# Optimization experiments

Hardware: AMD Instinct MI355X
Metric: run time of the kernel (lower is better)

The kernel has to match this reference:

```python
import jax, jax.numpy as jnp
import numpy as np
from jax import lax

SEQ, BS, D_IN, D_H, D_OUT, N_LAYERS = 784, 256, 1, 512, 1, 3

def _glorot(key, shape):
    fan_in, fan_out = shape[0], shape[1]
    std = jnp.sqrt(2.0 / (fan_in + fan_out))
    return (jax.random.normal(key, shape) * std).astype(jnp.float32)

def setup_inputs() -> dict:
    key = jax.random.key(0)
    ks = jax.random.split(key, 3 + 3 * N_LAYERS + 2)
    x = jax.random.normal(ks[0], (SEQ, BS, D_IN), dtype=jnp.float32)
    W0 = _glorot(ks[1], (D_IN, D_H))
    b0 = jnp.zeros((D_H,), jnp.float32)
    # per-layer recurrence params, stacked: a (L,D_H), B (L,D_H,D_H), C (L,D_H,D_H)
    a = jnp.stack([jax.random.uniform(ks[2 + i], (D_H,), minval=0.999, maxval=1.001) for i in range(N_LAYERS)]).astype(jnp.float32)
    B = jnp.stack([_glorot(ks[2 + N_LAYERS + i], (D_H, D_H)) for i in range(N_LAYERS)])
    C = jnp.stack([_glorot(ks[2 + 2 * N_LAYERS + i], (D_H, D_H)) for i in range(N_LAYERS)])
    Wf = _glorot(ks[2 + 3 * N_LAYERS], (D_H, D_OUT))
    bf = jnp.zeros((D_OUT,), jnp.float32)
    return {"x": x, "W0": W0, "b0": b0, "a": a, "B": B, "C": C, "Wf": Wf, "bf": bf}

def _rnn_layer(x, a_l, B_l, C_l):
    # x: (seq, bs, d_h); diagonal linear recurrence h_t = h_{t-1} * a + x_t @ B
    xb = jnp.einsum('sbi,ih->sbh', x, B_l)  # precompute input projection
    def step(h, xt):
        h = h * a_l + xt
        return h, h
    _, hs = lax.scan(step, jnp.zeros((x.shape[1], a_l.shape[0]), x.dtype), xb)
    return jnp.einsum('sbh,ho->sbo', hs, C_l)

def reference(x, W0, b0, a, B, C, Wf, bf):
    identity = x  # use_downsampling=False, use_residual=True
    h = jax.nn.relu(x @ W0 + b0)
    for l in range(N_LAYERS):
        h = jax.nn.relu(_rnn_layer(h, a[l], B[l], C[l]))
    out = h @ Wf + bf
    return out + identity
```

## Files before the change

kernel.cpp:

```cpp
#include <hip/hip_runtime.h>
#include <hip/hip_bf16.h>

#define SEQ 784
#define BS  256
#define DH  512
#define MT  (SEQ * BS)
#define NL  3
#define NC  14
#define CL  56
#define COLS (BS * DH)

typedef unsigned short u16;
typedef __bf16  bf16x8  __attribute__((ext_vector_type(8)));
typedef float   f32x4   __attribute__((ext_vector_type(4)));
typedef unsigned short u16x8 __attribute__((ext_vector_type(8)));
typedef unsigned short u16x4 __attribute__((ext_vector_type(4)));

__device__ __forceinline__ u16 f2b(float f) {
    unsigned int x = __float_as_uint(f);
    unsigned int r = (x + 0x7FFFu + ((x >> 16) & 1u)) >> 16;
    return (u16)r;
}
__device__ __forceinline__ float b2f(u16 u) {
    return __uint_as_float(((unsigned int)u) << 16);
}

__global__ __launch_bounds__(256) void prep_k(const float* __restrict__ B,
                                              const float* __restrict__ C,
                                              u16* __restrict__ Bp,
                                              u16* __restrict__ Cp)
{
    const long t = (long)blockIdx.x * 256 + threadIdx.x;
    const int  e  = (int)(t & 7);
    const int  l  = (int)((t >> 3) & 63);
    const int  ni = (int)((t >> 9) & 3);
    const int  wd = (int)((t >> 11) & 7);
    const int  g  = (int)((t >> 14) & 15);
    const long lay = t >> 18;
    const int  n = wd * 64 + ni * 16 + (l & 15);
    const int  k = g * 32 + (l >> 4) * 8 + e;
    const long src = (lay << 18) + (long)k * DH + n;
    Bp[t] = f2b(B[src]);
    Cp[t] = f2b(C[src]);
}


#define GEMM_STEP_KK(ATILE, tt)                                                  \
    _Pragma("unroll")                                                            \
    for (int kk = 0; kk < 2; ++kk) {                                             \
        bf16x8 bv[4];                                                            \
        _Pragma("unroll")                                                        \
        for (int ni = 0; ni < 4; ++ni)                                           \
            bv[ni] = *(const bf16x8*)&Wp[((long)((2 * (tt) + kk) * 32 +          \
                                                 wid * 4 + ni) << 9) +           \
                                         (lane << 3)];                           \
        const int fcol = ((kk * 4 + (lane >> 4)) ^ (lane & 7)) * 8;              \
        bf16x8 af[4];                                                            \
        _Pragma("unroll")                                                        \
        for (int i = 0; i < 4; ++i)                                              \
            af[i] = *(const bf16x8*)&(ATILE)[(i * 16 + (lane & 15)) * 64 + fcol];\
        _Pragma("unroll")                                                        \
        for (int mi = 0; mi < 4; ++mi)                                           \
            _Pragma("unroll")                                                    \
            for (int ni = 0; ni < 4; ++ni)                                       \
                acc[mi][ni] = __builtin_amdgcn_mfma_f32_16x16x32_bf16(           \
                    af[mi], bv[ni], acc[mi][ni], 0, 0, 0);                       \
    }

template <int RELU>
__global__ __launch_bounds__(512, 4) void gemm_ip(const u16* __restrict__ X,
                                                  const u16* __restrict__ Wp,
                                                  u16* __restrict__ Y)
{
    __shared__ __align__(16) u16 lds[64 * 512];

    const int tid  = threadIdx.x;
    const int lane = tid & 63;
    const int wid  = tid >> 6;
    const long bm  = (long)blockIdx.x * 64;

    const int srow = tid >> 3;
    const int scol = (((tid & 7) ^ (srow & 7)) * 8);
    const u16* gax = X + (bm + srow) * DH + scol;

    f32x4 acc[4][4];
#pragma unroll
    for (int i = 0; i < 4; ++i)
#pragma unroll
        for (int j = 0; j < 4; ++j)
            acc[i][j] = (f32x4){0.f, 0.f, 0.f, 0.f};

    __builtin_amdgcn_global_load_lds(
        (const __attribute__((address_space(1))) void*)gax,
        (__attribute__((address_space(3))) void*)
            ((__attribute__((address_space(3))) char*)lds + tid * 16),
        16, 0, 0);

    for (int t = 0; t < 8; ++t) {
        __syncthreads();
        if (t < 7) {
            __builtin_amdgcn_global_load_lds(
                (const __attribute__((address_space(1))) void*)(gax + (t + 1) * 64),
                (__attribute__((address_space(3))) void*)
                    ((__attribute__((address_space(3))) char*)lds +
                     ((t + 1) & 1) * 8192 + tid * 16),
                16, 0, 0);
        }
        const u16* Atile = lds + (t & 1) * 4096;
        GEMM_STEP_KK(Atile, t)
    }
    __syncthreads();

    u16* Ctile = lds;
    const int rbase = (lane >> 4) * 4;
    const int cloc  = wid * 64 + (lane & 15);
#pragma unroll
    for (int mi = 0; mi < 4; ++mi)
#pragma unroll
        for (int ni = 0; ni < 4; ++ni)
#pragma unroll
            for (int r = 0; r < 4; ++r) {
                float v = acc[mi][ni][r];
                if (RELU) v = fmaxf(v, 0.f);
                const int row = mi * 16 + rbase + r;
                const int col = (cloc + ni * 16) ^ (((row >> 2) & 3) * 16);
                Ctile[row * 512 + col] = f2b(v);
            }
    __syncthreads();
#pragma unroll
    for (int p = 0; p < 8; ++p) {
        const int e   = p * 4096 + tid * 8;
        const int row = e >> 9;
        const int col = e & 511;
        const int csw = col ^ (((row >> 2) & 3) * 16);
        *(u16x8*)&Y[(bm + row) * DH + col] = *(const u16x8*)&Ctile[row * 512 + csw];
    }
}

__global__ __launch_bounds__(512, 4) void gemm_first(const float* __restrict__ x,
                                                     const float* __restrict__ W0,
                                                     const float* __restrict__ b0,
                                                     const u16* __restrict__ Wp,
                                                     u16* __restrict__ Y)
{
    __shared__ __align__(16) u16 lds[64 * 512];

    const int tid  = threadIdx.x;
    const int lane = tid & 63;
    const int wid  = tid >> 6;
    const long bm  = (long)blockIdx.x * 64;

    const int prow = tid >> 3;
    const int slot = tid & 7;
    const float xv = x[bm + prow];

#pragma unroll
    for (int t = 0; t < 8; ++t) {
        const int k0 = t * 64 + ((slot ^ (prow & 7)) * 8);
        u16x8 o;
#pragma unroll
        for (int e = 0; e < 8; ++e)
            o[e] = f2b(fmaxf(fmaf(xv, W0[k0 + e], b0[k0 + e]), 0.f));
        *(u16x8*)&lds[t * 4096 + tid * 8] = o;
    }

    f32x4 acc[4][4];
#pragma unroll
    for (int i = 0; i < 4; ++i)
#pragma unroll
        for (int j = 0; j < 4; ++j)
            acc[i][j] = (f32x4){0.f, 0.f, 0.f, 0.f};

    __syncthreads();

#pragma unroll
    for (int t = 0; t < 8; ++t) {
        const u16* Atile = lds + t * 4096;
        GEMM_STEP_KK(Atile, t)
    }
    __syncthreads();

    u16* Ctile = lds;
    const int rbase = (lane >> 4) * 4;
    const int cloc  = wid * 64 + (lane & 15);
#pragma unroll
    for (int mi = 0; mi < 4; ++mi)
#pragma unroll
        for (int ni = 0; ni < 4; ++ni)
#pragma unroll
            for (int r = 0; r < 4; ++r) {
                const int row = mi * 16 + rbase + r;
                const int col = (cloc + ni * 16) ^ (((row >> 2) & 3) * 16);
                Ctile[row * 512 + col] = f2b(acc[mi][ni][r]);
            }
    __syncthreads();
#pragma unroll
    for (int p = 0; p < 8; ++p) {
        const int e   = p * 4096 + tid * 8;
        const int row = e >> 9;
        const int col = e & 511;
        const int csw = col ^ (((row >> 2) & 3) * 16);
        *(u16x8*)&Y[(bm + row) * DH + col] = *(const u16x8*)&Ctile[row * 512 + csw];
    }
}

__global__ __launch_bounds__(512, 4) void gemm_last(const u16* __restrict__ X,
                                                    const u16* __restrict__ Wp,
                                                    const float* __restrict__ Wf,
                                                    const float* __restrict__ bf_,
                                                    const float* __restrict__ x,
                                                    float* __restrict__ out)
{
    __shared__ __align__(16) u16 lds[64 * 512];
    float* partials = (float*)lds;

    const int tid  = threadIdx.x;
    const int lane = tid & 63;
    const int wid  = tid >> 6;
    const long bm  = (long)blockIdx.x * 64;

    const int srow = tid >> 3;
    const int scol = (((tid & 7) ^ (srow & 7)) * 8);
    const u16* gax = X + (bm + srow) * DH + scol;

    f32x4 acc[4][4];
#pragma unroll
    for (int i = 0; i < 4; ++i)
#pragma unroll
        for (int j = 0; j < 4; ++j)
            acc[i][j] = (f32x4){0.f, 0.f, 0.f, 0.f};

    __builtin_amdgcn_global_load_lds(
        (const __attribute__((address_space(1))) void*)gax,
        (__attribute__((address_space(3))) void*)
            ((__attribute__((address_space(3))) char*)lds + tid * 16),
        16, 0, 0);

    for (int t = 0; t < 8; ++t) {
        __syncthreads();
        if (t < 7) {
            __builtin_amdgcn_global_load_lds(
                (const __attribute__((address_space(1))) void*)(gax + (t + 1) * 64),
                (__attribute__((address_space(3))) void*)
                    ((__attribute__((address_space(3))) char*)lds +
                     ((t + 1) & 1) * 8192 + tid * 16),
                16, 0, 0);
        }
        const u16* Atile = lds + (t & 1) * 4096;
        GEMM_STEP_KK(Atile, t)
    }
    __syncthreads();

    const int cbase = wid * 64 + (lane & 15);
    float wf[4];
#pragma unroll
    for (int ni = 0; ni < 4; ++ni) wf[ni] = Wf[cbase + ni * 16];

    float part[4][4];
#pragma unroll
    for (int mi = 0; mi < 4; ++mi)
#pragma unroll
        for (int r = 0; r < 4; ++r) {
            float s = 0.f;
#pragma unroll
            for (int ni = 0; ni < 4; ++ni)
                s = fmaf(fmaxf(acc[mi][ni][r], 0.f), wf[ni], s);
            part[mi][r] = s;
        }
#pragma unroll
    for (int mi = 0; mi < 4; ++mi)
#pragma unroll
        for (int r = 0; r < 4; ++r) {
#pragma unroll
            for (int off = 1; off < 16; off <<= 1)
                part[mi][r] += __shfl_xor(part[mi][r], off, 64);
        }
    if ((lane & 15) == 0) {
        const int q = lane >> 4;
#pragma unroll
        for (int mi = 0; mi < 4; ++mi)
#pragma unroll
            for (int r = 0; r < 4; ++r)
                partials[wid * 64 + mi * 16 + q * 4 + r] = part[mi][r];
    }
    __syncthreads();
    if (tid < 64) {
        float s = 0.f;
#pragma unroll
        for (int w = 0; w < 8; ++w) s += partials[w * 64 + tid];
        out[bm + tid] = s + bf_[0] + x[bm + tid];
    }
}

__global__ __launch_bounds__(256) void scanA_k(const u16* __restrict__ buf,
                                               const float* __restrict__ a_all,
                                               int layer,
                                               float* __restrict__ carry)
{
    const long T   = (long)blockIdx.x * 256 + threadIdx.x;
    const int col4 = (int)(T & (COLS / 4 - 1)) * 4;
    const int c    = (int)(T >> 15);
    const f32x4 av = *(const f32x4*)&a_all[layer * DH + (col4 & (DH - 1))];
    const u16* p = buf + (long)c * CL * COLS + col4;

    float h[4] = {0.f, 0.f, 0.f, 0.f};
    u16x4 pre[8];
#pragma unroll
    for (int i = 0; i < 8; ++i) pre[i] = *(const u16x4*)&p[(long)i * COLS];
    for (int s8 = 0; s8 < CL; s8 += 8) {
        const bool more = (s8 + 8) < CL;
#pragma unroll
        for (int j = 0; j < 8; ++j) {
            const u16x4 v = pre[j];
            if (more) pre[j] = *(const u16x4*)&p[(long)(s8 + 8 + j) * COLS];
#pragma unroll
            for (int i = 0; i < 4; ++i)
                h[i] = fmaf(h[i], av[i], b2f((u16)v[i]));
        }
    }
    *(f32x4*)&carry[(long)c * COLS + col4] = (f32x4){h[0], h[1], h[2], h[3]};
}

__global__ __launch_bounds__(256) void scanC_k(u16* __restrict__ buf,
                                               const float* __restrict__ a_all,
                                               int layer,
                                               const float* __restrict__ carry)
{
    const long T   = (long)blockIdx.x * 256 + threadIdx.x;
    const int col4 = (int)(T & (COLS / 4 - 1)) * 4;
    const int c    = (int)(T >> 15);
    const f32x4 av = *(const f32x4*)&a_all[layer * DH + (col4 & (DH - 1))];
    u16* p = buf + (long)c * CL * COLS + col4;

    float h[4];
#pragma unroll
    for (int i = 0; i < 4; ++i) h[i] = 0.f;
    {
        float pw[4];
#pragma unroll
        for (int i = 0; i < 4; ++i) {
            float a2 = av[i] * av[i], a4 = a2 * a2, a8 = a4 * a4;
            float a16 = a8 * a8, a32 = a16 * a16;
            pw[i] = a32 * a16 * a8;
        }
        for (int cc = 0; cc < c; ++cc) {
            const f32x4 cr = *(const f32x4*)&carry[(long)cc * COLS + col4];
#pragma unroll
            for (int i = 0; i < 4; ++i)
                h[i] = fmaf(h[i], pw[i], cr[i]);
        }
    }

    u16x4 pre[8];
#pragma unroll
    for (int i = 0; i < 8; ++i) pre[i] = *(const u16x4*)&p[(long)i * COLS];
    for (int s8 = 0; s8 < CL; s8 += 8) {
        const bool more = (s8 + 8) < CL;
#pragma unroll
        for (int j = 0; j < 8; ++j) {
            const u16x4 v = pre[j];
            if (more) pre[j] = *(const u16x4*)&p[(long)(s8 + 8 + j) * COLS];
            u16x4 o;
#pragma unroll
            for (int i = 0; i < 4; ++i) {
                h[i] = fmaf(h[i], av[i], b2f((u16)v[i]));
                o[i] = f2b(h[i]);
            }
            *(u16x4*)&p[(long)(s8 + j) * COLS] = o;
        }
    }
}

extern "C" void kernel_launch(void* const* d_in, const int* in_sizes, int n_in,
                              void* d_out, int out_size, void* d_ws, size_t ws_size,
                              hipStream_t stream)
{
    const float* x   = (const float*)d_in[0];
    const float* W0  = (const float*)d_in[1];
    const float* b0  = (const float*)d_in[2];
    const float* a   = (const float*)d_in[3];
    const float* B   = (const float*)d_in[4];
    const float* C   = (const float*)d_in[5];
    const float* Wf  = (const float*)d_in[6];
    const float* bf_ = (const float*)d_in[7];
    float* out = (float*)d_out;

    const long BUF = (long)MT * DH;
    const size_t need = (size_t)BUF * 2 + 2ULL * 3 * DH * DH * 2
                      + (size_t)NC * COLS * 4;
    if (ws_size < need) return;

    u16*   buf   = (u16*)d_ws;
    u16*   Bp    = buf + BUF;
    u16*   Cp    = Bp + 3L * DH * DH;
    float* carry = (float*)(Cp + 3L * DH * DH);

    prep_k<<<(3 * DH * DH) / 256, 256, 0, stream>>>(B, C, Bp, Cp);

    for (int l = 0; l < NL; ++l) {
        if (l == 0)
            gemm_first<<<MT / 64, 512, 0, stream>>>(x, W0, b0, Bp, buf);
        else
            gemm_ip<0><<<MT / 64, 512, 0, stream>>>(buf, Bp + (long)l * DH * DH, buf);

        scanA_k<<<(NC * COLS / 4) / 256, 256, 0, stream>>>(buf, a, l, carry);
        scanC_k<<<(NC * COLS / 4) / 256, 256, 0, stream>>>(buf, a, l, carry);

        if (l == NL - 1)
            gemm_last<<<MT / 64, 512, 0, stream>>>(buf, Cp + (long)l * DH * DH,
                                                   Wf, bf_, x, out);
        else
            gemm_ip<1><<<MT / 64, 512, 0, stream>>>(buf, Cp + (long)l * DH * DH, buf);
    }
}
```

Measured before the change: 928.9 us.

## Fuse C-projection and next layer's B-projection GEMMs through LDS

Adds a gemm_dual kernel that computes relu(X@C_l) for a 64-row tile, keeps the bf16 result in shared memory, and immediately multiplies it by B_{l+1}. This replaces two separate GEMM launches between scans. It avoids writing and re-reading the full intermediate activation buffer through global memory. In exchange it uses more LDS per block and two accumulator sets, which may reduce occupancy. The shared k-loop and epilogue code is also turned into macros.

```diff
diff --git a/kernel.cpp b/kernel.cpp
--- a/kernel.cpp
+++ b/kernel.cpp
@@ -45,15 +45,15 @@
 }
 
 
-#define GEMM_STEP_KK(ATILE, tt)                                                  \
+#define GEMM_STEP_KK(ATILE, tt, ACC, WP)                                         \
     _Pragma("unroll")                                                            \
     for (int kk = 0; kk < 2; ++kk) {                                             \
         bf16x8 bv[4];                                                            \
         _Pragma("unroll")                                                        \
         for (int ni = 0; ni < 4; ++ni)                                           \
-            bv[ni] = *(const bf16x8*)&Wp[((long)((2 * (tt) + kk) * 32 +          \
-                                                 wid * 4 + ni) << 9) +           \
-                                         (lane << 3)];                           \
+            bv[ni] = *(const bf16x8*)&(WP)[((long)((2 * (tt) + kk) * 32 +        \
+                                                   wid * 4 + ni) << 9) +         \
+                                           (lane << 3)];                         \
         const int fcol = ((kk * 4 + (lane >> 4)) ^ (lane & 7)) * 8;              \
         bf16x8 af[4];                                                            \
         _Pragma("unroll")                                                        \
@@ -63,79 +63,58 @@
         for (int mi = 0; mi < 4; ++mi)                                           \
             _Pragma("unroll")                                                    \
             for (int ni = 0; ni < 4; ++ni)                                       \
-                acc[mi][ni] = __builtin_amdgcn_mfma_f32_16x16x32_bf16(           \
-                    af[mi], bv[ni], acc[mi][ni], 0, 0, 0);                       \
-    }
-
-template <int RELU>
-__global__ __launch_bounds__(512, 4) void gemm_ip(const u16* __restrict__ X,
-                                                  const u16* __restrict__ Wp,
-                                                  u16* __restrict__ Y)
-{
-    __shared__ __align__(16) u16 lds[64 * 512];
-
-    const int tid  = threadIdx.x;
-    const int lane = tid & 63;
-    const int wid  = tid >> 6;
-    const long bm  = (long)blockIdx.x * 64;
-
-    const int srow = tid >> 3;
-    const int scol = (((tid & 7) ^ (srow & 7)) * 8);
-    const u16* gax = X + (bm + srow) * DH + scol;
-
-    f32x4 acc[4][4];
-#pragma unroll
-    for (int i = 0; i < 4; ++i)
-#pragma unroll
-        for (int j = 0; j < 4; ++j)
-            acc[i][j] = (f32x4){0.f, 0.f, 0.f, 0.f};
-
-    __builtin_amdgcn_global_load_lds(
-        (const __attribute__((address_space(1))) void*)gax,
-        (__attribute__((address_space(3))) void*)
-            ((__attribute__((address_space(3))) char*)lds + tid * 16),
-        16, 0, 0);
-
-    for (int t = 0; t < 8; ++t) {
-        __syncthreads();
-        if (t < 7) {
-            __builtin_amdgcn_global_load_lds(
-                (const __attribute__((address_space(1))) void*)(gax + (t + 1) * 64),
-                (__attribute__((address_space(3))) void*)
-                    ((__attribute__((address_space(3))) char*)lds +
-                     ((t + 1) & 1) * 8192 + tid * 16),
-                16, 0, 0);
-        }
-        const u16* Atile = lds + (t & 1) * 4096;
-        GEMM_STEP_KK(Atile, t)
-    }
-    __syncthreads();
-
-    u16* Ctile = lds;
-    const int rbase = (lane >> 4) * 4;
-    const int cloc  = wid * 64 + (lane & 15);
-#pragma unroll
-    for (int mi = 0; mi < 4; ++mi)
-#pragma unroll
-        for (int ni = 0; ni < 4; ++ni)
-#pragma unroll
-            for (int r = 0; r < 4; ++r) {
-                float v = acc[mi][ni][r];
-                if (RELU) v = fmaxf(v, 0.f);
-                const int row = mi * 16 + rbase + r;
-                const int col = (cloc + ni * 16) ^ (((row >> 2) & 3) * 16);
-                Ctile[row * 512 + col] = f2b(v);
-            }
-    __syncthreads();
-#pragma unroll
-    for (int p = 0; p < 8; ++p) {
-        const int e   = p * 4096 + tid * 8;
-        const int row = e >> 9;
-        const int col = e & 511;
-        const int csw = col ^ (((row >> 2) & 3) * 16);
-        *(u16x8*)&Y[(bm + row) * DH + col] = *(const u16x8*)&Ctile[row * 512 + csw];
-    }
-}
+                (ACC)[mi][ni] = __builtin_amdgcn_mfma_f32_16x16x32_bf16(         \
+                    af[mi], bv[ni], (ACC)[mi][ni], 0, 0, 0);                     \
+    }
+
+#define GEMM_STAGED_KLOOP(ACC, WP)                                              \
+    __builtin_amdgcn_global_load_lds(                                           \
+        (const __attribute__((address_space(1))) void*)gax,                     \
+        (__attribute__((address_space(3))) void*)                               \
+            ((__attribute__((address_space(3))) char*)lds + tid * 16),          \
+        16, 0, 0);                                                              \
+    for (int t = 0; t < 8; ++t) {                                               \
+        __syncthreads();                                                        \
+        if (t < 7) {                                                            \
+            __builtin_amdgcn_global_load_lds(                                   \
+                (const __attribute__((address_space(1))) void*)(gax + (t + 1) * 64), \
+                (__attribute__((address_space(3))) void*)                       \
+                    ((__attribute__((address_space(3))) char*)lds +             \
+                     ((t + 1) & 1) * 8192 + tid * 16),                          \
+                16, 0, 0);                                                      \
+        }                                                                       \
+        const u16* Atile = lds + (t & 1) * 4096;                                \
+        GEMM_STEP_KK(Atile, t, ACC, WP)                                         \
+    }                                                                           \
+    __syncthreads();
+
+#define GEMM_C_EPILOGUE(CT, ACC, RELU_FLAG, DST)                                \
+    {                                                                           \
+        const int rbase = (lane >> 4) * 4;                                      \
+        const int cloc  = wid * 64 + (lane & 15);                               \
+        _Pragma("unroll")                                                       \
+        for (int mi = 0; mi < 4; ++mi)                                          \
+            _Pragma("unroll")                                                   \
+            for (int ni = 0; ni < 4; ++ni)                                      \
+                _Pragma("unroll")                                               \
+                for (int r = 0; r < 4; ++r) {                                   \
+                    float v = (ACC)[mi][ni][r];                                 \
+                    if (RELU_FLAG) v = fmaxf(v, 0.f);                           \
+                    const int row = mi * 16 + rbase + r;                        \
+                    const int col = (cloc + ni * 16) ^ (((row >> 2) & 3) * 16); \
+                    (CT)[row * 512 + col] = f2b(v);                             \
+                }                                                               \
+        __syncthreads();                                                        \
+        _Pragma("unroll")                                                       \
+        for (int p = 0; p < 8; ++p) {                                           \
+            const int e   = p * 4096 + tid * 8;                                 \
+            const int row = e >> 9;                                             \
+            const int col = e & 511;                                            \
+            const int csw = col ^ (((row >> 2) & 3) * 16);                      \
+            *(u16x8*)&(DST)[(bm + row) * DH + col] =                            \
+                *(const u16x8*)&(CT)[row * 512 + csw];                          \
+        }                                                                       \
+    }
 
 __global__ __launch_bounds__(512, 4) void gemm_first(const float* __restrict__ x,
                                                      const float* __restrict__ W0,
@@ -176,32 +155,73 @@
 #pragma unroll
     for (int t = 0; t < 8; ++t) {
         const u16* Atile = lds + t * 4096;
-        GEMM_STEP_KK(Atile, t)
+        GEMM_STEP_KK(Atile, t, acc, Wp)
     }
     __syncthreads();
 
     u16* Ctile = lds;
-    const int rbase = (lane >> 4) * 4;
-    const int cloc  = wid * 64 + (lane & 15);
-#pragma unroll
-    for (int mi = 0; mi < 4; ++mi)
-#pragma unroll
-        for (int ni = 0; ni < 4; ++ni)
-#pragma unroll
-            for (int r = 0; r < 4; ++r) {
-                const int row = mi * 16 + rbase + r;
-                const int col = (cloc + ni * 16) ^ (((row >> 2) & 3) * 16);
-                Ctile[row * 512 + col] = f2b(acc[mi][ni][r]);
+    GEMM_C_EPILOGUE(Ctile, acc, 0, Y)
+}
+
+__global__ __launch_bounds__(512, 4) void gemm_dual(const u16* __restrict__ X,
+                                                    const u16* __restrict__ WpC,
+                                                    const u16* __restrict__ WpB,
+                                                    u16* __restrict__ Yout)
+{
+    __shared__ __align__(16) u16 lds[8192 + 8 * 4096];
+
+    const int tid  = threadIdx.x;
+    const int lane = tid & 63;
+    const int wid  = tid >> 6;
+    const long bm  = (long)blockIdx.x * 64;
+
+    const int srow = tid >> 3;
+    const int scol = (((tid & 7) ^ (srow & 7)) * 8);
+    const u16* gax = X + (bm + srow) * DH + scol;
+
+    f32x4 acc[4][4];
+#pragma unroll
+    for (int i = 0; i < 4; ++i)
+#pragma unroll
+        for (int j = 0; j < 4; ++j)
+            acc[i][j] = (f32x4){0.f, 0.f, 0.f, 0.f};
+
+    GEMM_STAGED_KLOOP(acc, WpC)
+
+    u16* Yr = lds + 8192;
+    {
+        const int rbase = (lane >> 4) * 4;
+#pragma unroll
+        for (int mi = 0; mi < 4; ++mi)
+#pragma unroll
+            for (int ni = 0; ni < 4; ++ni) {
+                const int chunk = ni * 2 + ((lane & 15) >> 3);
+#pragma unroll
+                for (int r = 0; r < 4; ++r) {
+                    const int row = mi * 16 + rbase + r;
+                    Yr[wid * 4096 + row * 64 + ((chunk ^ (row & 7)) * 8) + (lane & 7)]
+                        = f2b(fmaxf(acc[mi][ni][r], 0.f));
+                }
             }
-    __syncthreads();
-#pragma unroll
-    for (int p = 0; p < 8; ++p) {
-        const int e   = p * 4096 + tid * 8;
-        const int row = e >> 9;
-        const int col = e & 511;
-        const int csw = col ^ (((row >> 2) & 3) * 16);
-        *(u16x8*)&Y[(bm + row) * DH + col] = *(const u16x8*)&Ctile[row * 512 + csw];
-    }
+    }
+    __syncthreads();
+
+    f32x4 acc2[4][4];
+#pragma unroll
+    for (int i = 0; i < 4; ++i)
+#pragma unroll
+        for (int j = 0; j < 4; ++j)
+            acc2[i][j] = (f32x4){0.f, 0.f, 0.f, 0.f};
+
+#pragma unroll
+    for (int t = 0; t < 8; ++t) {
+        const u16* Atile = Yr + t * 4096;
+        GEMM_STEP_KK(Atile, t, acc2, WpB)
+    }
+    __syncthreads();
+
+    u16* Ctile = Yr;
+    GEMM_C_EPILOGUE(Ctile, acc2, 0, Yout)
 }
 
 __global__ __launch_bounds__(512, 4) void gemm_last(const u16* __restrict__ X,
@@ -230,26 +250,7 @@
         for (int j = 0; j < 4; ++j)
             acc[i][j] = (f32x4){0.f, 0.f, 0.f, 0.f};
 
-    __builtin_amdgcn_global_load_lds(
-        (const __attribute__((address_space(1))) void*)gax,
-        (__attribute__((address_space(3))) void*)
-            ((__attribute__((address_space(3))) char*)lds + tid * 16),
-        16, 0, 0);
-
-    for (int t = 0; t < 8; ++t) {
-        __syncthreads();
-        if (t < 7) {
-            __builtin_amdgcn_global_load_lds(
-                (const __attribute__((address_space(1))) void*)(gax + (t + 1) * 64),
-                (__attribute__((address_space(3))) void*)
-                    ((__attribute__((address_space(3))) char*)lds +
-                     ((t + 1) & 1) * 8192 + tid * 16),
-                16, 0, 0);
-        }
-        const u16* Atile = lds + (t & 1) * 4096;
-        GEMM_STEP_KK(Atile, t)
-    }
-    __syncthreads();
+    GEMM_STAGED_KLOOP(acc, Wp)
 
     const int cbase = wid * 64 + (lane & 15);
     float wf[4];
@@ -397,19 +398,19 @@
 
     prep_k<<<(3 * DH * DH) / 256, 256, 0, stream>>>(B, C, Bp, Cp);
 
-    for (int l = 0; l < NL; ++l) {
-        if (l == 0)
-            gemm_first<<<MT / 64, 512, 0, stream>>>(x, W0, b0, Bp, buf);
-        else
-            gemm_ip<0><<<MT / 64, 512, 0, stream>>>(buf, Bp + (long)l * DH * DH, buf);
-
-        scanA_k<<<(NC * COLS / 4) / 256, 256, 0, stream>>>(buf, a, l, carry);
-        scanC_k<<<(NC * COLS / 4) / 256, 256, 0, stream>>>(buf, a, l, carry);
-
-        if (l == NL - 1)
-            gemm_last<<<MT / 64, 512, 0, stream>>>(buf, Cp + (long)l * DH * DH,
-                                                   Wf, bf_, x, out);
-        else
-            gemm_ip<1><<<MT / 64, 512, 0, stream>>>(buf, Cp + (long)l * DH * DH, buf);
-    }
-}
+    gemm_first<<<MT / 64, 512, 0, stream>>>(x, W0, b0, Bp, buf);
+    scanA_k<<<(NC * COLS / 4) / 256, 256, 0, stream>>>(buf, a, 0, carry);
+    scanC_k<<<(NC * COLS / 4) / 256, 256, 0, stream>>>(buf, a, 0, carry);
+
+    gemm_dual<<<MT / 64, 512, 0, stream>>>(buf, Cp, Bp + (long)DH * DH, buf);
+    scanA_k<<<(NC * COLS / 4) / 256, 256, 0, stream>>>(buf, a, 1, carry);
+    scanC_k<<<(NC * COLS / 4) / 256, 256, 0, stream>>>(buf, a, 1, carry);
+
+    gemm_dual<<<MT / 64, 512, 0, stream>>>(buf, Cp + (long)DH * DH,
+                                           Bp + 2L * DH * DH, buf);
+    scanA_k<<<(NC * COLS / 4) / 256, 256, 0, stream>>>(buf, a, 2, carry);
+    scanC_k<<<(NC * COLS / 4) / 256, 256, 0, stream>>>(buf, a, 2, carry);
+
+    gemm_last<<<MT / 64, 512, 0, stream>>>(buf, Cp + 2L * DH * DH,
+                                           Wf, bf_, x, out);
+}
```

After: 1.467 ms. 58.0% more time.
